# Optimization experiments

Hardware: AMD Instinct MI355X
Metric: run time of the kernel (lower is better)

Reference implementation:

```python
import jax, jax.numpy as jnp
import numpy as np

L, B, DW, DH, W, NG = 1024, 64, 300, 256, 2, 1
NEG = -1e25


def window_context(hx, w):
    """Concat of 2w+1 time-shifted copies of hx [L,B,D] -> [L,B,(2w+1)D].
    Order matches torch: shift-down by w..1, identity, shift-up by 1..w."""
    Lh = hx.shape[0]
    parts = []
    for i in range(w, -w - 1, -1):
        if i > 0:
            p = jnp.concatenate([jnp.zeros_like(hx[:i]), hx[:Lh - i]], axis=0)
        elif i < 0:
            k = -i
            p = jnp.concatenate([hx[k:], jnp.zeros_like(hx[:k])], axis=0)
        else:
            p = hx
        parts.append(p)
    return jnp.concatenate(parts, axis=2)


def setup_inputs() -> dict:
    key = jax.random.key(0)
    ks = jax.random.split(key, 11)
    E = (2 * W + 1) * DH
    std = 0.1  # reset_parameters('normal') uses N(0, 0.1)
    return {
        "src_seq": jax.random.normal(ks[0], (L, B, DW), jnp.float32),
        "h0": jax.random.normal(ks[1], (L + NG, B, DH), jnp.float32),
        "c0": jax.random.normal(ks[2], (L + NG, B, DH), jnp.float32),
        # word-gate params stacked over gates (i,l,r,f,s,o,u)
        "Ww": std * jax.random.normal(ks[3], (7, DH, E), jnp.float32),
        "Wu": std * jax.random.normal(ks[4], (7, DH, DW), jnp.float32),
        "Wv": std * jax.random.normal(ks[5], (7, DH, DH), jnp.float32),
        "Wb": std * jax.random.normal(ks[6], (7, DH), jnp.float32),
        # sentence-gate params stacked over gates (g,f,o)
        "Sw": std * jax.random.normal(ks[7], (3, DH, DH), jnp.float32),
        "Su": std * jax.random.normal(ks[8], (3, DH, DH), jnp.float32),
        "Sb": std * jax.random.normal(ks[9], (3, DH), jnp.float32),
        "src_len": jax.random.randint(ks[10], (B, 1), 1, L + 1, jnp.int32),
    }


def reference(src_seq, h0, c0, Ww, Wu, Wv, Wb, Sw, Su, Sb, src_len):
    # seq_mask[t, b] = True where t >= length[b]  -> [L, B, 1]
    seq_mask = (jnp.arange(L)[:, None] >= src_len[:, 0][None, :])[:, :, None]

    h_g1 = h0[L:]                                 # [1,B,DH] sentence node
    c_g1 = c0[L:]
    h_w1 = jnp.where(seq_mask, 0.0, h0[:L])       # [L,B,DH] word nodes
    c_w1 = jnp.where(seq_mask, 0.0, c0[:L])
    h_hat = h_w1.mean(axis=0)                     # [B,DH]
    hg = h_g1[0]                                  # [B,DH]

    # --- sentence node update (gate order g,f,o) ---
    fg = jax.nn.sigmoid(hg @ Sw[0].T + h_hat @ Su[0].T + Sb[0])[None]   # [1,B,DH]
    og = jax.nn.sigmoid(hg @ Sw[2].T + h_hat @ Su[2].T + Sb[2])[None]
    fi = jax.nn.sigmoid((hg @ Sw[1].T)[None]
                        + jnp.einsum('lbh,dh->lbd', h_w1, Su[1]) + Sb[1])
    fi = jnp.where(seq_mask, NEG, fi)
    fi_n = jax.nn.softmax(fi, axis=0)             # softmax over time
    c_g = fg * c_g1 + (fi_n * c_w1).sum(axis=0)
    h_g = og * jnp.tanh(c_g)

    # --- word node update (gate order i,l,r,f,s,o,u) ---
    eps = window_context(h_w1, W)                 # [L,B,(2W+1)DH]
    pre = (jnp.einsum('lbe,gde->glbd', eps, Ww)
           + jnp.einsum('lbw,gdw->glbd', src_seq, Wu)
           + jnp.einsum('bh,gdh->gbd', hg, Wv)[:, None]
           + Wb[:, None, None])                   # [7,L,B,DH]
    i_ = jax.nn.sigmoid(pre[0])
    l_ = jax.nn.sigmoid(pre[1])
    r_ = jax.nn.sigmoid(pre[2])
    f_ = jax.nn.sigmoid(pre[3])
    s_ = jax.nn.sigmoid(pre[4])
    o_ = jax.nn.sigmoid(pre[5])
    u_ = jnp.tanh(pre[6])

    gates = jnp.stack((l_, f_, r_, s_, i_), axis=0)          # [5,L,B,DH]
    gates = jnp.where(seq_mask[None], NEG, gates)
    gates_n = jax.nn.softmax(gates, axis=0)                  # softmax over 5 gates

    c_ctx = window_context(c_w1, 1)                          # window_size=1 (default)
    c_l, c_c, c_r = jnp.split(c_ctx, 3, axis=2)
    c_merged = jnp.stack(
        (c_l, c_c, c_r, jnp.broadcast_to(c_g1, c_c.shape), u_), axis=0)
    c_w = (gates_n * c_merged).sum(axis=0)
    c_w = jnp.where(seq_mask, 0.0, c_w)
    h_w = o_ * jnp.tanh(c_w)

    h_t = jnp.concatenate((h_w, h_g), axis=0)                # [L+1,B,DH]
    c_t = jnp.concatenate((c_w, c_g), axis=0)
    return (h_t, c_t)
```

## Files before the change

### kernel.cpp

```cpp
#include <hip/hip_runtime.h>
#include <hip/hip_bf16.h>

#define L_SEQ 1024
#define N_B   64
#define D_H   256
#define D_W   300
#define LDK   72
#define LDH   264

typedef __bf16 bf16x8 __attribute__((ext_vector_type(8)));
typedef float  f32x4  __attribute__((ext_vector_type(4)));
typedef unsigned short us8 __attribute__((ext_vector_type(8)));

#if defined(__has_builtin)
#if __has_builtin(__builtin_amdgcn_global_load_lds)
#define HAS_ASYNC_LDS 1
#endif
#endif

__device__ inline float b2f(unsigned short u){
    union { unsigned int i; float f; } v; v.i = ((unsigned int)u) << 16; return v.f;
}
__device__ inline unsigned short f2b(float f){
    union { float f; unsigned int i; } v; v.f = f;
    unsigned int u = v.i;
    return (unsigned short)((u + 0x7fffu + ((u >> 16) & 1u)) >> 16);
}
__device__ inline float sigf(float x){ return 1.0f / (1.0f + __expf(-x)); }
__device__ inline float tanhfast(float x){ return 1.0f - 2.0f / (__expf(2.0f*x) + 1.0f); }

__device__ inline float ldf(const void* p, size_t i, int isf){
    return isf ? ((const float*)p)[i] : b2f(((const unsigned short*)p)[i]);
}
__device__ inline unsigned short ld1b(const void* p, size_t i, int isf){
    return isf ? f2b(((const float*)p)[i]) : ((const unsigned short*)p)[i];
}
__device__ inline us8 ld8(const void* p, size_t i, int isf){
    if (isf){
        const float* f = (const float*)p + i;
        float4 x = *(const float4*)f;
        float4 y = *(const float4*)(f + 4);
        us8 r = { f2b(x.x), f2b(x.y), f2b(x.z), f2b(x.w),
                  f2b(y.x), f2b(y.y), f2b(y.z), f2b(y.w) };
        return r;
    }
    return *(const us8*)((const unsigned short*)p + i);
}
__device__ inline unsigned int ld2(const void* p, size_t i, int isf){
    if (isf){
        const float* f = (const float*)p + i;
        float2 x = *(const float2*)f;
        return (unsigned int)f2b(x.x) | ((unsigned int)f2b(x.y) << 16);
    }
    return *(const unsigned int*)((const unsigned short*)p + i);
}
__device__ inline float4 ldf4(const void* p, size_t i, int isf){
    if (isf) return *(const float4*)((const float*)p + i);
    unsigned long long v = *(const unsigned long long*)((const unsigned short*)p + i);
    float4 r;
    r.x = b2f((unsigned short)( v        & 0xffffu));
    r.y = b2f((unsigned short)((v >> 16) & 0xffffu));
    r.z = b2f((unsigned short)((v >> 32) & 0xffffu));
    r.w = b2f((unsigned short)( v >> 48));
    return r;
}

__device__ inline void stage16(const unsigned short* g, unsigned short* lds_base, int lane){
#ifdef HAS_ASYNC_LDS
    __builtin_amdgcn_global_load_lds(
        (const __attribute__((address_space(1))) unsigned int*)g,
        (__attribute__((address_space(3))) unsigned int*)lds_base, 16, 0, 0);
#else
    *(us8*)(lds_base + lane*8) = *(const us8*)g;
#endif
}

__global__ __launch_bounds__(256) void k_detect(const void* __restrict__ h0, int* __restrict__ flag)
{
    int tid = threadIdx.x;
    const unsigned short* u = (const unsigned short*)h0;
    int cnt = 0;
    #pragma unroll
    for (int i = 0; i < 4; i++){
        unsigned short v = u[(size_t)(tid * 4 + i) * 2];
        int e = (v >> 7) & 0xFF;
        cnt += (e >= 90 && e <= 150) ? 1 : 0;
    }
    __shared__ int red[256];
    red[tid] = cnt;
    __syncthreads();
    for (int s = 128; s > 0; s >>= 1){
        if (tid < s) red[tid] += red[tid + s];
        __syncthreads();
    }
    if (tid == 0) flag[0] = (red[0] > 512) ? 0 : 1;
}

__global__ __launch_bounds__(256) void k_conv_h(const void* __restrict__ h0,
    const int* __restrict__ slen, unsigned short* __restrict__ hpad, const int* __restrict__ flagp)
{
    int isf = flagp[0];
    int i = blockIdx.y;
    int idx = (blockIdx.x*256 + threadIdx.x)*8;
    int b = idx >> 8;
    int l = i - 2;
    us8 v = {0,0,0,0,0,0,0,0};
    if ((unsigned)l < 1024u && l < slen[b])
        v = ld8(h0, (size_t)l*16384 + idx, isf);
    *(us8*)(hpad + (size_t)i*16384 + idx) = v;
}

__global__ __launch_bounds__(256) void k_conv_src(const void* __restrict__ src,
    unsigned short* __restrict__ srcpad, const int* __restrict__ flagp)
{
    int isf = flagp[0];
    int gid = blockIdx.x*256 + threadIdx.x;
    int row = gid / 40, k = gid % 40, col = k*8;
    us8 v = {0,0,0,0,0,0,0,0};
    if (col + 8 <= 300) v = ld8(src, (size_t)row*300 + col, isf);
    else if (col < 300){
        for (int e = 0; e < 300 - col; ++e) v[e] = ld1b(src, (size_t)row*300 + col + e, isf);
    }
    *(us8*)(srcpad + (size_t)row*320 + col) = v;
}

__global__ __launch_bounds__(256) void k_conv_w(const void* __restrict__ Ww,
    const void* __restrict__ Wu, unsigned short* __restrict__ Wcat, const int* __restrict__ flagp)
{
    int isf = flagp[0];
    int gid = blockIdx.x*256 + threadIdx.x;
    int row = gid / 200, k = gid % 200, col = k*8;
    int dgrp = row / 112, rem = row % 112;
    int g = rem >> 4, d = dgrp*16 + (rem & 15);
    size_t n = (size_t)g*256 + d;
    us8 v = {0,0,0,0,0,0,0,0};
    if (col < 1280) v = ld8(Ww, n*1280 + col, isf);
    else {
        int w = col - 1280;
        if (w + 8 <= 300) v = ld8(Wu, n*300 + w, isf);
        else if (w < 300){
            for (int e = 0; e < 300 - w; ++e) v[e] = ld1b(Wu, n*300 + w + e, isf);
        }
    }
    *(us8*)(Wcat + (size_t)row*1600 + col) = v;
}

__global__ __launch_bounds__(256) void k_conv_su(const void* __restrict__ Su,
    unsigned short* __restrict__ Subf, const int* __restrict__ flagp)
{
    int isf = flagp[0];
    int gid = blockIdx.x*256 + threadIdx.x;
    *(us8*)(Subf + (size_t)gid*8) = ld8(Su, (size_t)65536 + (size_t)gid*8, isf);
}

__global__ __launch_bounds__(256) void k_hhat_fast(const unsigned short* __restrict__ hpad,
    float* __restrict__ hhat)
{
    int b = blockIdx.x, part = blockIdx.y, d = threadIdx.x;
    float s = 0.f;
    const unsigned short* p = hpad + (size_t)(2 + part*128)*16384 + b*256 + d;
    for (int ll = 0; ll < 128; ++ll)
        s += b2f(p[(size_t)ll*16384]);
    atomicAdd(&hhat[b*256 + d], s);
}

__global__ __launch_bounds__(1024) void k_hhat(const void* __restrict__ h0,
    const int* __restrict__ slen, float* __restrict__ hhat, const int* __restrict__ flagp)
{
    int isf = flagp[0];
    int b = blockIdx.x;
    int part = threadIdx.x >> 8;
    int d = threadIdx.x & 255;
    int lenb = slen[b];
    float s = 0.f;
    for (int l = part; l < lenb; l += 4)
        s += ldf(h0, (size_t)l*16384 + b*256 + d, isf);
    __shared__ float red[1024];
    red[threadIdx.x] = s;
    __syncthreads();
    if (part == 0)
        hhat[b*256 + d] = (red[d] + red[d+256] + red[d+512] + red[d+768]);
}

__global__ __launch_bounds__(256) void k_small(const void* __restrict__ h0,
    const float* __restrict__ hhat, const void* __restrict__ Sw,
    const void* __restrict__ Su, const void* __restrict__ Sb,
    float* __restrict__ fg, float* __restrict__ og, float* __restrict__ sg,
    const int* __restrict__ flagp, float hs)
{
    int isf = flagp[0];
    int b = blockIdx.x; int d = threadIdx.x;
    __shared__ float hgl[256], hhl[256];
    hgl[d] = ldf(h0, (size_t)16777216 + b*256 + d, isf);
    hhl[d] = hhat[b*256 + d] * hs;
    __syncthreads();
    size_t sw0 = (size_t)d*256, sw1 = (size_t)(256+d)*256, sw2 = (size_t)(512+d)*256;
    size_t su0 = (size_t)d*256, su2 = (size_t)(512+d)*256;
    float a0=0.f,a1=0.f,a2=0.f,a3=0.f,a4=0.f;
    #pragma unroll 4
    for (int h=0; h<256; h+=4){
        float4 w0 = ldf4(Sw, sw0+h, isf);
        float4 u0 = ldf4(Su, su0+h, isf);
        float4 w1 = ldf4(Sw, sw1+h, isf);
        float4 w2 = ldf4(Sw, sw2+h, isf);
        float4 u2 = ldf4(Su, su2+h, isf);
        float g0=hgl[h], g1=hgl[h+1], g2=hgl[h+2], g3=hgl[h+3];
        float q0=hhl[h], q1=hhl[h+1], q2=hhl[h+2], q3=hhl[h+3];
        a0 += g0*w0.x + g1*w0.y + g2*w0.z + g3*w0.w;
        a1 += q0*u0.x + q1*u0.y + q2*u0.z + q3*u0.w;
        a2 += g0*w1.x + g1*w1.y + g2*w1.z + g3*w1.w;
        a3 += g0*w2.x + g1*w2.y + g2*w2.z + g3*w2.w;
        a4 += q0*u2.x + q1*u2.y + q2*u2.z + q3*u2.w;
    }
    int i = b*256 + d;
    fg[i] = sigf(a0 + a1 + ldf(Sb, d, isf));
    sg[i] = a2 + ldf(Sb, 256 + d, isf);
    og[i] = sigf(a3 + a4 + ldf(Sb, 512 + d, isf));
}

__global__ __launch_bounds__(256) void k_hgwv(const void* __restrict__ h0,
    const void* __restrict__ Wv, const void* __restrict__ Wb,
    float* __restrict__ hgWvB, const int* __restrict__ flagp)
{
    int isf = flagp[0];
    int b = blockIdx.x, g = blockIdx.y, d = threadIdx.x;
    __shared__ float hgl[256];
    hgl[d] = ldf(h0, (size_t)16777216 + b*256 + d, isf);
    __syncthreads();
    size_t wv = ((size_t)g*256 + d)*256;
    float a = 0.f;
    #pragma unroll 4
    for (int h=0; h<256; h+=4){
        float4 w = ldf4(Wv, wv+h, isf);
        a += hgl[h]*w.x + hgl[h+1]*w.y + hgl[h+2]*w.z + hgl[h+3]*w.w;
    }
    hgWvB[(size_t)b*1792 + g*256 + d] = a + ldf(Wb, g*256 + d, isf);
}

__global__ __launch_bounds__(256) void k_fi_fast(const unsigned short* __restrict__ hpad,
    const void* __restrict__ c0, const unsigned short* __restrict__ Subf,
    const int* __restrict__ slen, const float* __restrict__ sg,
    float* __restrict__ numv, float* __restrict__ denv, const int* __restrict__ flagp)
{
    int isf = flagp[0];
    __shared__ unsigned short Hs[64*LDH];
    int tid = threadIdx.x;
    int b = blockIdx.x;
    int l0 = blockIdx.y * 64;
    int lenb = slen[b];
    #pragma unroll
    for (int i=0;i<8;i++){
        int c = tid + i*256;
        int r = c >> 5;
        int col = (c & 31) << 3;
        *(us8*)(Hs + r*LDH + col) =
            *(const us8*)(hpad + (size_t)(l0 + r + 2)*16384 + b*256 + col);
    }
    __syncthreads();
    int wv = tid >> 6, lane = tid & 63, qd = lane >> 4, lc = lane & 15;
    f32x4 zero4 = {0.f,0.f,0.f,0.f};
    for (int dci=0; dci<4; ++dci){
        int d = (wv*4 + dci) * 16 + lc;
        f32x4 acc[4];
        #pragma unroll
        for (int t=0;t<4;t++) acc[t] = zero4;
        #pragma unroll
        for (int ks=0; ks<8; ++ks){
            int k0 = ks*32 + qd*8;
            bf16x8 bb = *(const bf16x8*)(Subf + (size_t)d*256 + k0);
            #pragma unroll
            for (int lt=0; lt<4; ++lt){
                bf16x8 aa = *(const bf16x8*)(Hs + (lt*16 + lc)*LDH + k0);
                acc[lt] = __builtin_amdgcn_mfma_f32_16x16x32_bf16(aa, bb, acc[lt], 0, 0, 0);
            }
        }
        float sgv = sg[b*256 + d];
        float pn = 0.f, pd = 0.f;
        #pragma unroll
        for (int lt=0; lt<4; ++lt){
            #pragma unroll
            for (int r=0; r<4; ++r){
                int l = l0 + lt*16 + qd*4 + r;
                if (l < lenb){
                    float e = __expf(sigf(acc[lt][r] + sgv));
                    pd += e;
                    pn += e * ldf(c0, (size_t)l*16384 + b*256 + d, isf);
                }
            }
        }
        pn += __shfl_xor(pn, 16); pn += __shfl_xor(pn, 32);
        pd += __shfl_xor(pd, 16); pd += __shfl_xor(pd, 32);
        if (qd == 0){
            atomicAdd(&numv[b*256 + d], pn);
            atomicAdd(&denv[b*256 + d], pd);
        }
    }
}

__global__ __launch_bounds__(256) void k_fi(const void* __restrict__ h0,
    const void* __restrict__ c0, const void* __restrict__ Su,
    const int* __restrict__ slen, const float* __restrict__ sg,
    float* __restrict__ numv, float* __restrict__ denv, const int* __restrict__ flagp)
{
    int isf = flagp[0];
    __shared__ unsigned short Hs[64*LDH];
    int tid = threadIdx.x;
    int b = blockIdx.x;
    int l0 = blockIdx.y * 64;
    int lenb = slen[b];
    #pragma unroll
    for (int i=0;i<8;i++){
        int c = tid + i*256;
        int r = c >> 5;
        int col = (c & 31) << 3;
        int l = l0 + r;
        us8 v = {0,0,0,0,0,0,0,0};
        if (l < lenb)
            v = ld8(h0, (size_t)l*16384 + b*256 + col, isf);
        *(us8*)(Hs + r*LDH + col) = v;
    }
    __syncthreads();
    int wv = tid >> 6, lane = tid & 63, qd = lane >> 4, lc = lane & 15;
    f32x4 zero4 = {0.f,0.f,0.f,0.f};
    for (int dci=0; dci<4; ++dci){
        int d = (wv*4 + dci) * 16 + lc;
        f32x4 acc[4];
        #pragma unroll
        for (int t=0;t<4;t++) acc[t] = zero4;
        #pragma unroll
        for (int ks=0; ks<8; ++ks){
            int k0 = ks*32 + qd*8;
            union { us8 u; bf16x8 b; } cv; cv.u = ld8(Su, (size_t)65536 + (size_t)d*256 + k0, isf);
            bf16x8 bb = cv.b;
            #pragma unroll
            for (int lt=0; lt<4; ++lt){
                bf16x8 aa = *(const bf16x8*)(Hs + (lt*16 + lc)*LDH + k0);
                acc[lt] = __builtin_amdgcn_mfma_f32_16x16x32_bf16(aa, bb, acc[lt], 0, 0, 0);
            }
        }
        float sgv = sg[b*256 + d];
        float pn = 0.f, pd = 0.f;
        #pragma unroll
        for (int lt=0; lt<4; ++lt){
            #pragma unroll
            for (int r=0; r<4; ++r){
                int l = l0 + lt*16 + qd*4 + r;
                if (l < lenb){
                    float e = __expf(sigf(acc[lt][r] + sgv));
                    pd += e;
                    pn += e * ldf(c0, (size_t)l*16384 + b*256 + d, isf);
                }
            }
        }
        pn += __shfl_xor(pn, 16); pn += __shfl_xor(pn, 32);
        pd += __shfl_xor(pd, 16); pd += __shfl_xor(pd, 32);
        if (qd == 0){
            atomicAdd(&numv[b*256 + d], pn);
            atomicAdd(&denv[b*256 + d], pd);
        }
    }
}

__global__ __launch_bounds__(256) void k_cg(const void* __restrict__ c0,
    const float* __restrict__ fg, const float* __restrict__ og,
    const float* __restrict__ numv, const float* __restrict__ denv,
    float* __restrict__ outh, float* __restrict__ outc,
    const int* __restrict__ flagp)
{
    int isf = flagp[0];
    int i = blockIdx.x*256 + threadIdx.x;
    float cg1 = ldf(c0, (size_t)16777216 + i, isf);
    float cg = fg[i]*cg1 + numv[i]/denv[i];
    float hg = og[i]*tanhfast(cg);
    outh[(size_t)16777216 + i] = hg;
    outc[(size_t)16777216 + i] = cg;
}

__global__ __launch_bounds__(256) void k_main_fast(
    const unsigned short* __restrict__ hpad, const unsigned short* __restrict__ srcpad,
    const unsigned short* __restrict__ Wcat, const void* __restrict__ c0,
    const int* __restrict__ slen, const float* __restrict__ hgWvB,
    float* __restrict__ outh, float* __restrict__ outc, const int* __restrict__ flagp)
{
    int isf = flagp[0];
    __shared__ unsigned short As[2][128*64];
    __shared__ unsigned short Bs[2][112*64];
    int tid = threadIdx.x;
    int d0 = blockIdx.x * 16;
    int m0 = blockIdx.y * 128;
    int wv = tid >> 6, lane = tid & 63, qd = lane >> 4, lc = lane & 15;

    const unsigned short* gbB = Wcat + (size_t)blockIdx.x * 112 * 1600;

    int arow[4], agc[4];
    #pragma unroll
    for (int i=0;i<4;i++){
        int s = i*256 + tid;
        arow[i] = s >> 3;
        agc[i]  = ((s & 7) ^ ((s >> 3) & 7)) << 3;
    }
    int s3 = 768 + tid;
    int brow3 = s3 >> 3;
    int bgc3  = ((s3 & 7) ^ ((s3 >> 3) & 7)) << 3;

    f32x4 zero4 = {0.f,0.f,0.f,0.f};
    f32x4 acc[2][7];
    #pragma unroll
    for (int a=0;a<2;a++)
        #pragma unroll
        for (int g=0;g<7;g++) acc[a][g] = zero4;

#define STAGE_TILE(sel_, kt_) do {                                                   \
        const unsigned short* ga_; int astr_;                                        \
        if ((kt_) < 20){                                                             \
            ga_ = hpad + (((size_t)(m0 + (((kt_)>>2)<<6))) << 8) + (((kt_) & 3) << 6); \
            astr_ = 256;                                                             \
        } else {                                                                     \
            ga_ = srcpad + (size_t)m0*320 + (((kt_) - 20) << 6);                     \
            astr_ = 320;                                                             \
        }                                                                            \
        const unsigned short* gb_ = gbB + ((size_t)(kt_) << 6);                      \
        _Pragma("unroll")                                                            \
        for (int i_=0;i_<4;i_++)                                                     \
            stage16(ga_ + (size_t)arow[i_]*astr_ + agc[i_],                          \
                    &As[(sel_)][i_*2048 + wv*512], lane);                            \
        _Pragma("unroll")                                                            \
        for (int i_=0;i_<3;i_++)                                                     \
            stage16(gb_ + (size_t)arow[i_]*1600 + agc[i_],                           \
                    &Bs[(sel_)][i_*2048 + wv*512], lane);                            \
        if (tid < 128)                                                               \
            stage16(gb_ + (size_t)brow3*1600 + bgc3,                                 \
                    &Bs[(sel_)][3*2048 + wv*512], lane);                             \
    } while(0)

    STAGE_TILE(0, 0);
    asm volatile("s_waitcnt vmcnt(0)" ::: "memory");
    __builtin_amdgcn_s_barrier();
    asm volatile("" ::: "memory");

    int cur = 0;
    for (int kt=0; kt<25; ++kt){
        if (kt < 24){
            int nxt = cur ^ 1;
            int kk  = kt + 1;
            STAGE_TILE(nxt, kk);
        }
        const unsigned short* Ac = &As[cur][0];
        const unsigned short* Bc = &Bs[cur][0];
        __builtin_amdgcn_s_setprio(1);
        #pragma unroll
        for (int ks=0; ks<2; ++ks){
            int ch = (ks << 2) + qd;
            int xa = (ch ^ (lc & 7)) << 3;
            bf16x8 a0 = *(const bf16x8*)(Ac + (wv*32 + lc)*64 + xa);
            bf16x8 a1 = *(const bf16x8*)(Ac + (wv*32 + 16 + lc)*64 + xa);
            #pragma unroll
            for (int g=0; g<7; ++g){
                bf16x8 bg = *(const bf16x8*)(Bc + (g*16 + lc)*64 + xa);
                acc[0][g] = __builtin_amdgcn_mfma_f32_16x16x32_bf16(a0, bg, acc[0][g], 0,0,0);
                acc[1][g] = __builtin_amdgcn_mfma_f32_16x16x32_bf16(a1, bg, acc[1][g], 0,0,0);
            }
        }
        __builtin_amdgcn_s_setprio(0);
        asm volatile("s_waitcnt vmcnt(0) lgkmcnt(0)" ::: "memory");
        __builtin_amdgcn_s_barrier();
        asm volatile("" ::: "memory");
        cur ^= 1;
    }
#undef STAGE_TILE

    int d = d0 + lc;
    #pragma unroll
    for (int mt=0; mt<2; ++mt){
        #pragma unroll
        for (int r=0; r<4; ++r){
            int m = m0 + wv*32 + mt*16 + qd*4 + r;
            int l = m >> 6, b = m & 63;
            size_t oi = (size_t)m*256 + d;
            int lenb = slen[b];
            float hw = 0.f, cw = 0.f;
            if (l < lenb){
                const float* hv = hgWvB + (size_t)b*1792 + d;
                float p0 = acc[mt][0][r] + hv[0];
                float p1 = acc[mt][1][r] + hv[256];
                float p2 = acc[mt][2][r] + hv[512];
                float p3 = acc[mt][3][r] + hv[768];
                float p4 = acc[mt][4][r] + hv[1024];
                float p5 = acc[mt][5][r] + hv[1280];
                float p6 = acc[mt][6][r] + hv[1536];
                float e_l = __expf(sigf(p1));
                float e_f = __expf(sigf(p3));
                float e_r = __expf(sigf(p2));
                float e_s = __expf(sigf(p4));
                float e_i = __expf(sigf(p0));
                float S = e_l + e_f + e_r + e_s + e_i;
                float u_ = tanhfast(p6);
                float cl = (l >= 1) ? ldf(c0, oi - 16384, isf) : 0.f;
                float cc = ldf(c0, oi, isf);
                float cr = (l + 1 < lenb) ? ldf(c0, oi + 16384, isf) : 0.f;
                float cg1 = ldf(c0, (size_t)16777216 + b*256 + d, isf);
                cw = (e_l*cl + e_f*cc + e_r*cr + e_s*cg1 + e_i*u_) / S;
                hw = sigf(p5) * tanhfast(cw);
            }
            outh[oi] = hw;
            outc[oi] = cw;
        }
    }
}

__global__ __launch_bounds__(256) void k_main(
    const void* __restrict__ src, const void* __restrict__ h0,
    const void* __restrict__ c0, const void* __restrict__ Ww,
    const void* __restrict__ Wu, const int* __restrict__ slen,
    const float* __restrict__ hgWvB,
    float* __restrict__ outh, float* __restrict__ outc,
    const int* __restrict__ flagp)
{
    int isf = flagp[0];
    __shared__ unsigned short As[128*LDK];
    __shared__ unsigned short Bs[112*LDK];
    int tid = threadIdx.x;
    int m0 = blockIdx.x * 128;
    int d0 = blockIdx.y * 16;
    int wv = tid >> 6, lane = tid & 63, qd = lane >> 4, lc = lane & 15;

    int ar[4], acol[4], al[4], ab[4], alen[4];
    #pragma unroll
    for (int i=0;i<4;i++){
        int c = tid + i*256;
        ar[i] = c >> 3; acol[i] = (c & 7) << 3;
        int m = m0 + ar[i];
        al[i] = m >> 6; ab[i] = m & 63;
        alen[i] = slen[ab[i]];
    }

    f32x4 zero4 = {0.f,0.f,0.f,0.f};
    f32x4 acc[2][7];
    #pragma unroll
    for (int a=0;a<2;a++)
        #pragma unroll
        for (int g=0;g<7;g++) acc[a][g] = zero4;

    for (int kt=0; kt<25; ++kt){
        __syncthreads();
        if (kt < 20){
            int j = kt >> 2;
            int koff = (kt & 3) << 6;
            #pragma unroll
            for (int i=0;i<4;i++){
                int lp = al[i] + j - 2;
                us8 v = {0,0,0,0,0,0,0,0};
                if ((unsigned)lp < 1024u && lp < alen[i])
                    v = ld8(h0, (size_t)lp*16384 + ab[i]*256 + koff + acol[i], isf);
                *(us8*)(As + ar[i]*LDK + acol[i]) = v;
            }
            #pragma unroll
            for (int i=0;i<4;i++){
                int c = tid + i*256;
                if (c < 896){
                    int rr = c >> 3, col = (c & 7) << 3;
                    int g = rr >> 4, d = d0 + (rr & 15);
                    *(us8*)(Bs + rr*LDK + col) =
                        ld8(Ww, ((size_t)g*256 + d)*1280 + j*256 + koff + col, isf);
                }
            }
        } else {
            int w0 = (kt - 20) << 6;
            #pragma unroll
            for (int i=0;i<16;i++){
                int c = tid + i*256;
                int r = c >> 5, wi = (c & 31) << 1;
                int w = w0 + wi;
                int m = m0 + r;
                unsigned int v = 0;
                if (w < 300) v = ld2(src, (size_t)m*300 + w, isf);
                *(unsigned int*)(As + r*LDK + wi) = v;
            }
            #pragma unroll
            for (int i=0;i<14;i++){
                int c = tid + i*256;
                int rr = c >> 5, wi = (c & 31) << 1;
                int w = w0 + wi;
                int g = rr >> 4, d = d0 + (rr & 15);
                unsigned int v = 0;
                if (w < 300) v = ld2(Wu, ((size_t)g*256 + d)*300 + w, isf);
                *(unsigned int*)(Bs + rr*LDK + wi) = v;
            }
        }
        __syncthreads();
        #pragma unroll
        for (int ks=0; ks<2; ++ks){
            int k0 = (ks << 5) + (qd << 3);
            bf16x8 a0 = *(const bf16x8*)(As + (wv*32 + lc)*LDK + k0);
            bf16x8 a1 = *(const bf16x8*)(As + (wv*32 + 16 + lc)*LDK + k0);
            #pragma unroll
            for (int g=0; g<7; ++g){
                bf16x8 bg = *(const bf16x8*)(Bs + (g*16 + lc)*LDK + k0);
                acc[0][g] = __builtin_amdgcn_mfma_f32_16x16x32_bf16(a0, bg, acc[0][g], 0,0,0);
                acc[1][g] = __builtin_amdgcn_mfma_f32_16x16x32_bf16(a1, bg, acc[1][g], 0,0,0);
            }
        }
    }

    int d = d0 + lc;
    #pragma unroll
    for (int mt=0; mt<2; ++mt){
        #pragma unroll
        for (int r=0; r<4; ++r){
            int m = m0 + wv*32 + mt*16 + qd*4 + r;
            int l = m >> 6, b = m & 63;
            size_t oi = (size_t)m*256 + d;
            int lenb = slen[b];
            float hw = 0.f, cw = 0.f;
            if (l < lenb){
                const float* hv = hgWvB + (size_t)b*1792 + d;
                float p0 = acc[mt][0][r] + hv[0];
                float p1 = acc[mt][1][r] + hv[256];
                float p2 = acc[mt][2][r] + hv[512];
                float p3 = acc[mt][3][r] + hv[768];
                float p4 = acc[mt][4][r] + hv[1024];
                float p5 = acc[mt][5][r] + hv[1280];
                float p6 = acc[mt][6][r] + hv[1536];
                float e_l = __expf(sigf(p1));
                float e_f = __expf(sigf(p3));
                float e_r = __expf(sigf(p2));
                float e_s = __expf(sigf(p4));
                float e_i = __expf(sigf(p0));
                float S = e_l + e_f + e_r + e_s + e_i;
                float u_ = tanhfast(p6);
                float cl = (l >= 1) ? ldf(c0, oi - 16384, isf) : 0.f;
                float cc = ldf(c0, oi, isf);
                float cr = (l + 1 < lenb) ? ldf(c0, oi + 16384, isf) : 0.f;
                float cg1 = ldf(c0, (size_t)16777216 + b*256 + d, isf);
                cw = (e_l*cl + e_f*cc + e_r*cr + e_s*cg1 + e_i*u_) / S;
                hw = sigf(p5) * tanhfast(cw);
            }
            outh[oi] = hw;
            outc[oi] = cw;
        }
    }
}

extern "C" void kernel_launch(void* const* d_in, const int* in_sizes, int n_in,
                              void* d_out, int out_size, void* d_ws, size_t ws_size,
                              hipStream_t stream)
{
    const void* src = d_in[0];
    const void* h0  = d_in[1];
    const void* c0  = d_in[2];
    const void* Ww  = d_in[3];
    const void* Wu  = d_in[4];
    const void* Wv  = d_in[5];
    const void* Wb  = d_in[6];
    const void* Sw  = d_in[7];
    const void* Su  = d_in[8];
    const void* Sb  = d_in[9];
    const int* slen = (const int*)d_in[10];

    float* outh = (float*)d_out;
    float* outc = outh + (size_t)1025*64*256;

    float* ws    = (float*)d_ws;
    float* numv  = ws;
    float* denv  = ws + 16384;
    float* hhat  = ws + 32768;
    float* fg    = ws + 49152;
    float* og    = ws + 65536;
    float* sg    = ws + 81920;
    float* hgWvB = ws + 98304;
    int*   flag  = (int*)(ws + 212992);

    unsigned short* bfbase = (unsigned short*)(ws + 213024);
    unsigned short* hpad   = bfbase;
    unsigned short* srcpad = bfbase + (size_t)16842752;
    unsigned short* Wcat   = bfbase + (size_t)37814272;
    unsigned short* Subf   = bfbase + (size_t)40681472;
    const size_t NEED = 852096 + (size_t)40747008*2;

    hipLaunchKernelGGL(k_detect, dim3(1), dim3(256), 0, stream, h0, flag);
    hipMemsetAsync(ws, 0, (size_t)3*16384*sizeof(float), stream);

    if (ws_size >= NEED){
        hipLaunchKernelGGL(k_conv_h,  dim3(8,1028), dim3(256), 0, stream, h0, slen, hpad, flag);
        hipLaunchKernelGGL(k_conv_src, dim3(10240), dim3(256), 0, stream, src, srcpad, flag);
        hipLaunchKernelGGL(k_conv_w,   dim3(1400),  dim3(256), 0, stream, Ww, Wu, Wcat, flag);
        hipLaunchKernelGGL(k_conv_su,  dim3(32),    dim3(256), 0, stream, Su, Subf, flag);
        hipLaunchKernelGGL(k_hhat_fast, dim3(64,8), dim3(256), 0, stream, hpad, hhat);
        hipLaunchKernelGGL(k_small, dim3(64), dim3(256), 0, stream, h0, hhat, Sw, Su, Sb,
                           fg, og, sg, flag, 1.0f/1024.0f);
        hipLaunchKernelGGL(k_hgwv, dim3(64,7), dim3(256), 0, stream, h0, Wv, Wb, hgWvB, flag);
        hipLaunchKernelGGL(k_fi_fast, dim3(64,16), dim3(256), 0, stream, hpad, c0, Subf, slen,
                           sg, numv, denv, flag);
        hipLaunchKernelGGL(k_cg, dim3(64), dim3(256), 0, stream, c0, fg, og, numv, denv,
                           outh, outc, flag);
        hipLaunchKernelGGL(k_main_fast, dim3(16,512), dim3(256), 0, stream,
                           hpad, srcpad, Wcat, c0, slen, hgWvB, outh, outc, flag);
    } else {
        hipLaunchKernelGGL(k_hhat, dim3(64), dim3(1024), 0, stream, h0, slen, hhat, flag);
        hipLaunchKernelGGL(k_small, dim3(64), dim3(256), 0, stream, h0, hhat, Sw, Su, Sb,
                           fg, og, sg, flag, 1.0f/1024.0f);
        hipLaunchKernelGGL(k_hgwv, dim3(64,7), dim3(256), 0, stream, h0, Wv, Wb, hgWvB, flag);
        hipLaunchKernelGGL(k_fi, dim3(64,16), dim3(256), 0, stream, h0, c0, Su, slen,
                           sg, numv, denv, flag);
        hipLaunchKernelGGL(k_cg, dim3(64), dim3(256), 0, stream, c0, fg, og, numv, denv,
                           outh, outc, flag);
        hipLaunchKernelGGL(k_main, dim3(512,16), dim3(256), 0, stream,
                           src, h0, c0, Ww, Wu, slen, hgWvB, outh, outc, flag);
    }
}
```

Before: 976.9 us.

## Restructure main GEMM to 4-stage 32-wide K pipeline with partial vmcnt waits

```diff
diff --git a/kernel.cpp b/kernel.cpp
--- a/kernel.cpp
+++ b/kernel.cpp
@@ -383,25 +383,43 @@
     float* __restrict__ outh, float* __restrict__ outc, const int* __restrict__ flagp)
 {
     int isf = flagp[0];
-    __shared__ unsigned short As[2][128*64];
-    __shared__ unsigned short Bs[2][112*64];
+    __shared__ unsigned short smem[32768];
     int tid = threadIdx.x;
     int d0 = blockIdx.x * 16;
     int m0 = blockIdx.y * 128;
     int wv = tid >> 6, lane = tid & 63, qd = lane >> 4, lc = lane & 15;
 
-    const unsigned short* gbB = Wcat + (size_t)blockIdx.x * 112 * 1600;
-
-    int arow[4], agc[4];
-    #pragma unroll
-    for (int i=0;i<4;i++){
-        int s = i*256 + tid;
-        arow[i] = s >> 3;
-        agc[i]  = ((s & 7) ^ ((s >> 3) & 7)) << 3;
-    }
-    int s3 = 768 + tid;
-    int brow3 = s3 >> 3;
-    int bgc3  = ((s3 & 7) ^ ((s3 >> 3) & 7)) << 3;
+    const unsigned short* gBbase = Wcat + (size_t)blockIdx.x * 112 * 1600;
+    const unsigned short* gAh = hpad + (size_t)m0 * 256;
+    const unsigned short* gAs = srcpad + (size_t)m0 * 320;
+
+    int goffAh[2], goffAs[2], goffB[2];
+    #pragma unroll
+    for (int i=0;i<2;i++){
+        int c = i*256 + tid;
+        int r = c >> 2, sl = c & 3;
+        int mk = (r & 3) ^ ((r >> 2) & 3);
+        int gc = sl ^ mk;
+        goffAh[i] = r*256 + (gc<<3);
+        goffAs[i] = r*320 + (gc<<3);
+        int rb = (r < 112) ? r : 111;
+        goffB[i]  = rb*1600 + (gc<<3);
+    }
+
+    int r0 = wv*32 + lc, r1 = r0 + 16;
+    int aoff0 = r0*32 + ((qd ^ ((r0&3)^((r0>>2)&3))) << 3);
+    int aoff1 = r1*32 + ((qd ^ ((r1&3)^((r1>>2)&3))) << 3);
+    int boff0, boff1, boff2, boff3, boff4, boff5, boff6;
+    {
+        int rb, mk;
+        rb = 0*16+lc; mk = (rb&3)^((rb>>2)&3); boff0 = 4096 + rb*32 + ((qd^mk)<<3);
+        rb = 1*16+lc; mk = (rb&3)^((rb>>2)&3); boff1 = 4096 + rb*32 + ((qd^mk)<<3);
+        rb = 2*16+lc; mk = (rb&3)^((rb>>2)&3); boff2 = 4096 + rb*32 + ((qd^mk)<<3);
+        rb = 3*16+lc; mk = (rb&3)^((rb>>2)&3); boff3 = 4096 + rb*32 + ((qd^mk)<<3);
+        rb = 4*16+lc; mk = (rb&3)^((rb>>2)&3); boff4 = 4096 + rb*32 + ((qd^mk)<<3);
+        rb = 5*16+lc; mk = (rb&3)^((rb>>2)&3); boff5 = 4096 + rb*32 + ((qd^mk)<<3);
+        rb = 6*16+lc; mk = (rb&3)^((rb>>2)&3); boff6 = 4096 + rb*32 + ((qd^mk)<<3);
+    }
 
     f32x4 zero4 = {0.f,0.f,0.f,0.f};
     f32x4 acc[2][7];
@@ -410,64 +428,75 @@
         #pragma unroll
         for (int g=0;g<7;g++) acc[a][g] = zero4;
 
-#define STAGE_TILE(sel_, kt_) do {                                                   \
-        const unsigned short* ga_; int astr_;                                        \
-        if ((kt_) < 20){                                                             \
-            ga_ = hpad + (((size_t)(m0 + (((kt_)>>2)<<6))) << 8) + (((kt_) & 3) << 6); \
-            astr_ = 256;                                                             \
-        } else {                                                                     \
-            ga_ = srcpad + (size_t)m0*320 + (((kt_) - 20) << 6);                     \
-            astr_ = 320;                                                             \
-        }                                                                            \
-        const unsigned short* gb_ = gbB + ((size_t)(kt_) << 6);                      \
-        _Pragma("unroll")                                                            \
-        for (int i_=0;i_<4;i_++)                                                     \
-            stage16(ga_ + (size_t)arow[i_]*astr_ + agc[i_],                          \
-                    &As[(sel_)][i_*2048 + wv*512], lane);                            \
-        _Pragma("unroll")                                                            \
-        for (int i_=0;i_<3;i_++)                                                     \
-            stage16(gb_ + (size_t)arow[i_]*1600 + agc[i_],                           \
-                    &Bs[(sel_)][i_*2048 + wv*512], lane);                            \
-        if (tid < 128)                                                               \
-            stage16(gb_ + (size_t)brow3*1600 + bgc3,                                 \
-                    &Bs[(sel_)][3*2048 + wv*512], lane);                             \
+#define STAGE_H(hs_) do {                                                        \
+        int hh_ = (hs_);                                                         \
+        unsigned short* sb_ = smem + (hh_&3)*8192;                               \
+        const unsigned short* gB_ = gBbase + hh_*32;                             \
+        if (hh_ < 40){                                                           \
+            const unsigned short* gA_ = gAh + ((hh_>>3)*16384 + ((hh_&7)<<5));   \
+            stage16(gA_ + goffAh[0], sb_ + wv*512, lane);                        \
+            stage16(gA_ + goffAh[1], sb_ + 2048 + wv*512, lane);                 \
+        } else {                                                                 \
+            const unsigned short* gA_ = gAs + ((hh_-40)<<5);                     \
+            stage16(gA_ + goffAs[0], sb_ + wv*512, lane);                        \
+            stage16(gA_ + goffAs[1], sb_ + 2048 + wv*512, lane);                 \
+        }                                                                        \
+        stage16(gB_ + goffB[0], sb_ + 4096 + wv*512, lane);                      \
+        stage16(gB_ + goffB[1], sb_ + 6144 + wv*512, lane);                      \
     } while(0)
 
-    STAGE_TILE(0, 0);
-    asm volatile("s_waitcnt vmcnt(0)" ::: "memory");
+#define ITER_H(h_, DS_) do {                                                     \
+        const unsigned short* lb_ = smem + ((h_)&3)*8192;                        \
+        bf16x8 va0 = *(const bf16x8*)(lb_ + aoff0);                              \
+        bf16x8 va1 = *(const bf16x8*)(lb_ + aoff1);                              \
+        bf16x8 vb0 = *(const bf16x8*)(lb_ + boff0);                              \
+        bf16x8 vb1 = *(const bf16x8*)(lb_ + boff1);                              \
+        bf16x8 vb2 = *(const bf16x8*)(lb_ + boff2);                              \
+        bf16x8 vb3 = *(const bf16x8*)(lb_ + boff3);                              \
+        bf16x8 vb4 = *(const bf16x8*)(lb_ + boff4);                              \
+        bf16x8 vb5 = *(const bf16x8*)(lb_ + boff5);                              \
+        bf16x8 vb6 = *(const bf16x8*)(lb_ + boff6);                              \
+        if (DS_) STAGE_H((h_) + 3);                                              \
+        __builtin_amdgcn_s_setprio(1);                                           \
+        acc[0][0] = __builtin_amdgcn_mfma_f32_16x16x32_bf16(va0, vb0, acc[0][0],0,0,0); \
+        acc[1][0] = __builtin_amdgcn_mfma_f32_16x16x32_bf16(va1, vb0, acc[1][0],0,0,0); \
+        acc[0][1] = __builtin_amdgcn_mfma_f32_16x16x32_bf16(va0, vb1, acc[0][1],0,0,0); \
+        acc[1][1] = __builtin_amdgcn_mfma_f32_16x16x32_bf16(va1, vb1, acc[1][1],0,0,0); \
+        acc[0][2] = __builtin_amdgcn_mfma_f32_16x16x32_bf16(va0, vb2, acc[0][2],0,0,0); \
+        acc[1][2] = __builtin_amdgcn_mfma_f32_16x16x32_bf16(va1, vb2, acc[1][2],0,0,0); \
+        acc[0][3] = __builtin_amdgcn_mfma_f32_16x16x32_bf16(va0, vb3, acc[0][3],0,0,0); \
+        acc[1][3] = __builtin_amdgcn_mfma_f32_16x16x32_bf16(va1, vb3, acc[1][3],0,0,0); \
+        acc[0][4] = __builtin_amdgcn_mfma_f32_16x16x32_bf16(va0, vb4, acc[0][4],0,0,0); \
+        acc[1][4] = __builtin_amdgcn_mfma_f32_16x16x32_bf16(va1, vb4, acc[1][4],0,0,0); \
+        acc[0][5] = __builtin_amdgcn_mfma_f32_16x16x32_bf16(va0, vb5, acc[0][5],0,0,0); \
+        acc[1][5] = __builtin_amdgcn_mfma_f32_16x16x32_bf16(va1, vb5, acc[1][5],0,0,0); \
+        acc[0][6] = __builtin_amdgcn_mfma_f32_16x16x32_bf16(va0, vb6, acc[0][6],0,0,0); \
+        acc[1][6] = __builtin_amdgcn_mfma_f32_16x16x32_bf16(va1, vb6, acc[1][6],0,0,0); \
+        __builtin_amdgcn_s_setprio(0);                                           \
+    } while(0)
+
+    STAGE_H(0); STAGE_H(1); STAGE_H(2);
+    asm volatile("s_waitcnt vmcnt(8)" ::: "memory");
     __builtin_amdgcn_s_barrier();
     asm volatile("" ::: "memory");
 
-    int cur = 0;
-    for (int kt=0; kt<25; ++kt){
-        if (kt < 24){
-            int nxt = cur ^ 1;
-            int kk  = kt + 1;
-            STAGE_TILE(nxt, kk);
-        }
-        const unsigned short* Ac = &As[cur][0];
-        const unsigned short* Bc = &Bs[cur][0];
-        __builtin_amdgcn_s_setprio(1);
-        #pragma unroll
-        for (int ks=0; ks<2; ++ks){
-            int ch = (ks << 2) + qd;
-            int xa = (ch ^ (lc & 7)) << 3;
-            bf16x8 a0 = *(const bf16x8*)(Ac + (wv*32 + lc)*64 + xa);
-            bf16x8 a1 = *(const bf16x8*)(Ac + (wv*32 + 16 + lc)*64 + xa);
-            #pragma unroll
-            for (int g=0; g<7; ++g){
-                bf16x8 bg = *(const bf16x8*)(Bc + (g*16 + lc)*64 + xa);
-                acc[0][g] = __builtin_amdgcn_mfma_f32_16x16x32_bf16(a0, bg, acc[0][g], 0,0,0);
-                acc[1][g] = __builtin_amdgcn_mfma_f32_16x16x32_bf16(a1, bg, acc[1][g], 0,0,0);
-            }
-        }
-        __builtin_amdgcn_s_setprio(0);
-        asm volatile("s_waitcnt vmcnt(0) lgkmcnt(0)" ::: "memory");
+    for (int h = 0; h < 47; ++h){
+        ITER_H(h, 1);
+        asm volatile("s_waitcnt vmcnt(8) lgkmcnt(0)" ::: "memory");
         __builtin_amdgcn_s_barrier();
         asm volatile("" ::: "memory");
-        cur ^= 1;
-    }
-#undef STAGE_TILE
+    }
+    ITER_H(47, 0);
+    asm volatile("s_waitcnt vmcnt(4) lgkmcnt(0)" ::: "memory");
+    __builtin_amdgcn_s_barrier();
+    asm volatile("" ::: "memory");
+    ITER_H(48, 0);
+    asm volatile("s_waitcnt vmcnt(0) lgkmcnt(0)" ::: "memory");
+    __builtin_amdgcn_s_barrier();
+    asm volatile("" ::: "memory");
+    ITER_H(49, 0);
+#undef ITER_H
+#undef STAGE_H
 
     int d = d0 + lc;
     #pragma unroll
```

Measured after the change: 945.2 us. 3.2% less time.

## Pre-pack weights into MFMA fragment order and load GEMM operands directly to registers

Applied to the files above, without the earlier changes.

```diff
diff --git a/kernel.cpp b/kernel.cpp
--- a/kernel.cpp
+++ b/kernel.cpp
@@ -65,16 +65,6 @@
     return r;
 }
 
-__device__ inline void stage16(const unsigned short* g, unsigned short* lds_base, int lane){
-#ifdef HAS_ASYNC_LDS
-    __builtin_amdgcn_global_load_lds(
-        (const __attribute__((address_space(1))) unsigned int*)g,
-        (__attribute__((address_space(3))) unsigned int*)lds_base, 16, 0, 0);
-#else
-    *(us8*)(lds_base + lane*8) = *(const us8*)g;
-#endif
-}
-
 __global__ __launch_bounds__(256) void k_detect(const void* __restrict__ h0, int* __restrict__ flag)
 {
     int tid = threadIdx.x;
@@ -129,20 +119,22 @@
 {
     int isf = flagp[0];
     int gid = blockIdx.x*256 + threadIdx.x;
-    int row = gid / 200, k = gid % 200, col = k*8;
-    int dgrp = row / 112, rem = row % 112;
-    int g = rem >> 4, d = dgrp*16 + (rem & 15);
+    int bx = gid / 22400, rem = gid % 22400;
+    int h = rem / 448, rem2 = rem % 448;
+    int rr = rem2 >> 2, c8 = rem2 & 3;
+    int g = rr >> 4, d = bx*16 + (rr & 15);
+    int k = h*32 + c8*8;
     size_t n = (size_t)g*256 + d;
     us8 v = {0,0,0,0,0,0,0,0};
-    if (col < 1280) v = ld8(Ww, n*1280 + col, isf);
+    if (k < 1280) v = ld8(Ww, n*1280 + k, isf);
     else {
-        int w = col - 1280;
+        int w = k - 1280;
         if (w + 8 <= 300) v = ld8(Wu, n*300 + w, isf);
         else if (w < 300){
             for (int e = 0; e < 300 - w; ++e) v[e] = ld1b(Wu, n*300 + w + e, isf);
         }
     }
-    *(us8*)(Wcat + (size_t)row*1600 + col) = v;
+    *(us8*)(Wcat + (size_t)gid*8) = v;
 }
 
 __global__ __launch_bounds__(256) void k_conv_su(const void* __restrict__ Su,
@@ -376,32 +368,156 @@
     outc[(size_t)16777216 + i] = cg;
 }
 
-__global__ __launch_bounds__(256) void k_main_fast(
+__global__ __launch_bounds__(256, 2) void k_main_fast(
     const unsigned short* __restrict__ hpad, const unsigned short* __restrict__ srcpad,
     const unsigned short* __restrict__ Wcat, const void* __restrict__ c0,
     const int* __restrict__ slen, const float* __restrict__ hgWvB,
     float* __restrict__ outh, float* __restrict__ outc, const int* __restrict__ flagp)
 {
     int isf = flagp[0];
-    __shared__ unsigned short As[2][128*64];
-    __shared__ unsigned short Bs[2][112*64];
     int tid = threadIdx.x;
     int d0 = blockIdx.x * 16;
-    int m0 = blockIdx.y * 128;
+    int m0 = blockIdx.y * 256;
     int wv = tid >> 6, lane = tid & 63, qd = lane >> 4, lc = lane & 15;
 
-    const unsigned short* gbB = Wcat + (size_t)blockIdx.x * 112 * 1600;
-
-    int arow[4], agc[4];
+    int mr0 = m0 + wv*64 + lc;
+    const unsigned short* pA0h = hpad + (size_t)(mr0      )*256 + qd*8;
+    const unsigned short* pA1h = hpad + (size_t)(mr0 + 16 )*256 + qd*8;
+    const unsigned short* pA2h = hpad + (size_t)(mr0 + 32 )*256 + qd*8;
+    const unsigned short* pA3h = hpad + (size_t)(mr0 + 48 )*256 + qd*8;
+    const unsigned short* pA0s = srcpad + (size_t)(mr0      )*320 + qd*8;
+    const unsigned short* pA1s = srcpad + (size_t)(mr0 + 16 )*320 + qd*8;
+    const unsigned short* pA2s = srcpad + (size_t)(mr0 + 32 )*320 + qd*8;
+    const unsigned short* pA3s = srcpad + (size_t)(mr0 + 48 )*320 + qd*8;
+    const unsigned short* pB = Wcat + ((size_t)(blockIdx.x*50)*112 + lc)*32 + qd*8;
+
+    f32x4 zero4 = {0.f,0.f,0.f,0.f};
+    f32x4 acc[4][7];
+    #pragma unroll
+    for (int a=0;a<4;a++)
+        #pragma unroll
+        for (int g=0;g<7;g++) acc[a][g] = zero4;
+
+#define LOAD_PH(AV, BV, h_) do {                                                 \
+        int hh_ = (h_);                                                          \
+        if (hh_ < 40){                                                           \
+            int off_ = ((hh_>>3)<<14) + ((hh_&7)<<5);                            \
+            AV##0 = *(const bf16x8*)(pA0h + off_);                               \
+            AV##1 = *(const bf16x8*)(pA1h + off_);                               \
+            AV##2 = *(const bf16x8*)(pA2h + off_);                               \
+            AV##3 = *(const bf16x8*)(pA3h + off_);                               \
+        } else {                                                                 \
+            int off_ = (hh_ - 40) << 5;                                          \
+            AV##0 = *(const bf16x8*)(pA0s + off_);                               \
+            AV##1 = *(const bf16x8*)(pA1s + off_);                               \
+            AV##2 = *(const bf16x8*)(pA2s + off_);                               \
+            AV##3 = *(const bf16x8*)(pA3s + off_);                               \
+        }                                                                        \
+        const unsigned short* bp_ = pB + hh_*3584;                               \
+        BV##0 = *(const bf16x8*)(bp_ + 0);                                       \
+        BV##1 = *(const bf16x8*)(bp_ + 512);                                     \
+        BV##2 = *(const bf16x8*)(bp_ + 1024);                                    \
+        BV##3 = *(const bf16x8*)(bp_ + 1536);                                    \
+        BV##4 = *(const bf16x8*)(bp_ + 2048);                                    \
+        BV##5 = *(const bf16x8*)(bp_ + 2560);                                    \
+        BV##6 = *(const bf16x8*)(bp_ + 3072);                                    \
+    } while(0)
+
+#define MG1(A_, B_, g_) do {                                                     \
+        acc[0][g_] = __builtin_amdgcn_mfma_f32_16x16x32_bf16(A_##0, B_##g_, acc[0][g_],0,0,0); \
+        acc[1][g_] = __builtin_amdgcn_mfma_f32_16x16x32_bf16(A_##1, B_##g_, acc[1][g_],0,0,0); \
+        acc[2][g_] = __builtin_amdgcn_mfma_f32_16x16x32_bf16(A_##2, B_##g_, acc[2][g_],0,0,0); \
+        acc[3][g_] = __builtin_amdgcn_mfma_f32_16x16x32_bf16(A_##3, B_##g_, acc[3][g_],0,0,0); \
+    } while(0)
+#define MFMA_PH(A_, B_) do { MG1(A_,B_,0); MG1(A_,B_,1); MG1(A_,B_,2); MG1(A_,B_,3); \
+                             MG1(A_,B_,4); MG1(A_,B_,5); MG1(A_,B_,6); } while(0)
+
+    bf16x8 xa0, xa1, xa2, xa3, ya0, ya1, ya2, ya3;
+    bf16x8 xb0, xb1, xb2, xb3, xb4, xb5, xb6;
+    bf16x8 yb0, yb1, yb2, yb3, yb4, yb5, yb6;
+
+    LOAD_PH(xa, xb, 0);
+    for (int h = 0; h < 48; h += 2){
+        LOAD_PH(ya, yb, h+1);
+        __builtin_amdgcn_s_setprio(1);
+        MFMA_PH(xa, xb);
+        __builtin_amdgcn_s_setprio(0);
+        LOAD_PH(xa, xb, h+2);
+        __builtin_amdgcn_s_setprio(1);
+        MFMA_PH(ya, yb);
+        __builtin_amdgcn_s_setprio(0);
+    }
+    LOAD_PH(ya, yb, 49);
+    MFMA_PH(xa, xb);
+    MFMA_PH(ya, yb);
+#undef LOAD_PH
+#undef MG1
+#undef MFMA_PH
+
+    int d = d0 + lc;
+    #pragma unroll
+    for (int mt=0; mt<4; ++mt){
+        #pragma unroll
+        for (int r=0; r<4; ++r){
+            int m = m0 + wv*64 + mt*16 + qd*4 + r;
+            int l = m >> 6, b = m & 63;
+            size_t oi = (size_t)m*256 + d;
+            int lenb = slen[b];
+            float hw = 0.f, cw = 0.f;
+            if (l < lenb){
+                const float* hv = hgWvB + (size_t)b*1792 + d;
+                float p0 = acc[mt][0][r] + hv[0];
+                float p1 = acc[mt][1][r] + hv[256];
+                float p2 = acc[mt][2][r] + hv[512];
+                float p3 = acc[mt][3][r] + hv[768];
+                float p4 = acc[mt][4][r] + hv[1024];
+                float p5 = acc[mt][5][r] + hv[1280];
+                float p6 = acc[mt][6][r] + hv[1536];
+                float e_l = __expf(sigf(p1));
+                float e_f = __expf(sigf(p3));
+                float e_r = __expf(sigf(p2));
+                float e_s = __expf(sigf(p4));
+                float e_i = __expf(sigf(p0));
+                float S = e_l + e_f + e_r + e_s + e_i;
+                float u_ = tanhfast(p6);
+                float cl = (l >= 1) ? ldf(c0, oi - 16384, isf) : 0.f;
+                float cc = ldf(c0, oi, isf);
+                float cr = (l + 1 < lenb) ? ldf(c0, oi + 16384, isf) : 0.f;
+                float cg1 = ldf(c0, (size_t)16777216 + b*256 + d, isf);
+                cw = (e_l*cl + e_f*cc + e_r*cr + e_s*cg1 + e_i*u_) / S;
+                hw = sigf(p5) * tanhfast(cw);
+            }
+            outh[oi] = hw;
+            outc[oi] = cw;
+        }
+    }
+}
+
+__global__ __launch_bounds__(256) void k_main(
+    const void* __restrict__ src, const void* __restrict__ h0,
+    const void* __restrict__ c0, const void* __restrict__ Ww,
+    const void* __restrict__ Wu, const int* __restrict__ slen,
+    const float* __restrict__ hgWvB,
+    float* __restrict__ outh, float* __restrict__ outc,
+    const int* __restrict__ flagp)
+{
+    int isf = flagp[0];
+    __shared__ unsigned short As[128*LDK];
+    __shared__ unsigned short Bs[112*LDK];
+    int tid = threadIdx.x;
+    int m0 = blockIdx.x * 128;
+    int d0 = blockIdx.y * 16;
+    int wv = tid >> 6, lane = tid & 63, qd = lane >> 4, lc = lane & 15;
+
+    int ar[4], acol[4], al[4], ab[4], alen[4];
     #pragma unroll
     for (int i=0;i<4;i++){
-        int s = i*256 + tid;
-        arow[i] = s >> 3;
-        agc[i]  = ((s & 7) ^ ((s >> 3) & 7)) << 3;
-    }
-    int s3 = 768 + tid;
-    int brow3 = s3 >> 3;
-    int bgc3  = ((s3 & 7) ^ ((s3 >> 3) & 7)) << 3;
+        int c = tid + i*256;
+        ar[i] = c >> 3; acol[i] = (c & 7) << 3;
+        int m = m0 + ar[i];
+        al[i] = m >> 6; ab[i] = m & 63;
+        alen[i] = slen[ab[i]];
+    }
 
     f32x4 zero4 = {0.f,0.f,0.f,0.f};
     f32x4 acc[2][7];
@@ -410,64 +526,66 @@
         #pragma unroll
         for (int g=0;g<7;g++) acc[a][g] = zero4;
 
-#define STAGE_TILE(sel_, kt_) do {                                                   \
-        const unsigned short* ga_; int astr_;                                        \
-        if ((kt_) < 20){                                                             \
-            ga_ = hpad + (((size_t)(m0 + (((kt_)>>2)<<6))) << 8) + (((kt_) & 3) << 6); \
-            astr_ = 256;                                                             \
-        } else {                                                                     \
-            ga_ = srcpad + (size_t)m0*320 + (((kt_) - 20) << 6);                     \
-            astr_ = 320;                                                             \
-        }                                                                            \
-        const unsigned short* gb_ = gbB + ((size_t)(kt_) << 6);                      \
-        _Pragma("unroll")                                                            \
-        for (int i_=0;i_<4;i_++)                                                     \
-            stage16(ga_ + (size_t)arow[i_]*astr_ + agc[i_],                          \
-                    &As[(sel_)][i_*2048 + wv*512], lane);                            \
-        _Pragma("unroll")                                                            \
-        for (int i_=0;i_<3;i_++)                                                     \
-            stage16(gb_ + (size_t)arow[i_]*1600 + agc[i_],                           \
-                    &Bs[(sel_)][i_*2048 + wv*512], lane);                            \
-        if (tid < 128)                                                               \
-            stage16(gb_ + (size_t)brow3*1600 + bgc3,                                 \
-                    &Bs[(sel_)][3*2048 + wv*512], lane);                             \
-    } while(0)
-
-    STAGE_TILE(0, 0);
-    asm volatile("s_waitcnt vmcnt(0)" ::: "memory");
-    __builtin_amdgcn_s_barrier();
-    asm volatile("" ::: "memory");
-
-    int cur = 0;
     for (int kt=0; kt<25; ++kt){
-        if (kt < 24){
-            int nxt = cur ^ 1;
-            int kk  = kt + 1;
-            STAGE_TILE(nxt, kk);
-        }
-        const unsigned short* Ac = &As[cur][0];
-        const unsigned short* Bc = &Bs[cur][0];
-        __builtin_amdgcn_s_setprio(1);
+        __syncthreads();
+        if (kt < 20){
+            int j = kt >> 2;
+            int koff = (kt & 3) << 6;
+            #pragma unroll
+            for (int i=0;i<4;i++){
+                int lp = al[i] + j - 2;
+                us8 v = {0,0,0,0,0,0,0,0};
+                if ((unsigned)lp < 1024u && lp < alen[i])
+                    v = ld8(h0, (size_t)lp*16384 + ab[i]*256 + koff + acol[i], isf);
+                *(us8*)(As + ar[i]*LDK + acol[i]) = v;
+            }
+            #pragma unroll
+            for (int i=0;i<4;i++){
+                int c = tid + i*256;
+                if (c < 896){
+                    int rr = c >> 3, col = (c & 7) << 3;
+                    int g = rr >> 4, d = d0 + (rr & 15);
+                    *(us8*)(Bs + rr*LDK + col) =
+                        ld8(Ww, ((size_t)g*256 + d)*1280 + j*256 + koff + col, isf);
+                }
+            }
+        } else {
+            int w0 = (kt - 20) << 6;
+            #pragma unroll
+            for (int i=0;i<16;i++){
+                int c = tid + i*256;
+                int r = c >> 5, wi = (c & 31) << 1;
+                int w = w0 + wi;
+                int m = m0 + r;
+                unsigned int v = 0;
+                if (w < 300) v = ld2(src, (size_t)m*300 + w, isf);
+                *(unsigned int*)(As + r*LDK + wi) = v;
+            }
+            #pragma unroll
+            for (int i=0;i<14;i++){
+                int c = tid + i*256;
+                int rr = c >> 5, wi = (c & 31) << 1;
+                int w = w0 + wi;
+                int g = rr >> 4, d = d0 + (rr & 15);
+                unsigned int v = 0;
+                if (w < 300) v = ld2(Wu, ((size_t)g*256 + d)*300 + w, isf);
+                *(unsigned int*)(Bs + rr*LDK + wi) = v;
+            }
+        }
+        __syncthreads();
         #pragma unroll
         for (int ks=0; ks<2; ++ks){
-            int ch = (ks << 2) + qd;
-            int xa = (ch ^ (lc & 7)) << 3;
-            bf16x8 a0 = *(const bf16x8*)(Ac + (wv*32 + lc)*64 + xa);
-            bf16x8 a1 = *(const bf16x8*)(Ac + (wv*32 + 16 + lc)*64 + xa);
+            int k0 = (ks << 5) + (qd << 3);
+            bf16x8 a0 = *(const bf16x8*)(As + (wv*32 + lc)*LDK + k0);
+            bf16x8 a1 = *(const bf16x8*)(As + (wv*32 + 16 + lc)*LDK + k0);
             #pragma unroll
             for (int g=0; g<7; ++g){
-                bf16x8 bg = *(const bf16x8*)(Bc + (g*16 + lc)*64 + xa);
+                bf16x8 bg = *(const bf16x8*)(Bs + (g*16 + lc)*LDK + k0);
                 acc[0][g] = __builtin_amdgcn_mfma_f32_16x16x32_bf16(a0, bg, acc[0][g], 0,0,0);
                 acc[1][g] = __builtin_amdgcn_mfma_f32_16x16x32_bf16(a1, bg, acc[1][g], 0,0,0);
             }
         }
-        __builtin_amdgcn_s_setprio(0);
-        asm volatile("s_waitcnt vmcnt(0) lgkmcnt(0)" ::: "memory");
-        __builtin_amdgcn_s_barrier();
-        asm volatile("" ::: "memory");
-        cur ^= 1;
-    }
-#undef STAGE_TILE
+    }
 
     int d = d0 + lc;
     #pragma unroll
@@ -508,139 +626,6 @@
     }
 }
 
-__global__ __launch_bounds__(256) void k_main(
-    const void* __restrict__ src, const void* __restrict__ h0,
-    const void* __restrict__ c0, const void* __restrict__ Ww,
-    const void* __restrict__ Wu, const int* __restrict__ slen,
-    const float* __restrict__ hgWvB,
-    float* __restrict__ outh, float* __restrict__ outc,
-    const int* __restrict__ flagp)
-{
-    int isf = flagp[0];
-    __shared__ unsigned short As[128*LDK];
-    __shared__ unsigned short Bs[112*LDK];
-    int tid = threadIdx.x;
-    int m0 = blockIdx.x * 128;
-    int d0 = blockIdx.y * 16;
-    int wv = tid >> 6, lane = tid & 63, qd = lane >> 4, lc = lane & 15;
-
-    int ar[4], acol[4], al[4], ab[4], alen[4];
-    #pragma unroll
-    for (int i=0;i<4;i++){
-        int c = tid + i*256;
-        ar[i] = c >> 3; acol[i] = (c & 7) << 3;
-        int m = m0 + ar[i];
-        al[i] = m >> 6; ab[i] = m & 63;
-        alen[i] = slen[ab[i]];
-    }
-
-    f32x4 zero4 = {0.f,0.f,0.f,0.f};
-    f32x4 acc[2][7];
-    #pragma unroll
-    for (int a=0;a<2;a++)
-        #pragma unroll
-        for (int g=0;g<7;g++) acc[a][g] = zero4;
-
-    for (int kt=0; kt<25; ++kt){
-        __syncthreads();
-        if (kt < 20){
-            int j = kt >> 2;
-            int koff = (kt & 3) << 6;
-            #pragma unroll
-            for (int i=0;i<4;i++){
-                int lp = al[i] + j - 2;
-                us8 v = {0,0,0,0,0,0,0,0};
-                if ((unsigned)lp < 1024u && lp < alen[i])
-                    v = ld8(h0, (size_t)lp*16384 + ab[i]*256 + koff + acol[i], isf);
-                *(us8*)(As + ar[i]*LDK + acol[i]) = v;
-            }
-            #pragma unroll
-            for (int i=0;i<4;i++){
-                int c = tid + i*256;
-                if (c < 896){
-                    int rr = c >> 3, col = (c & 7) << 3;
-                    int g = rr >> 4, d = d0 + (rr & 15);
-                    *(us8*)(Bs + rr*LDK + col) =
-                        ld8(Ww, ((size_t)g*256 + d)*1280 + j*256 + koff + col, isf);
-                }
-            }
-        } else {
-            int w0 = (kt - 20) << 6;
-            #pragma unroll
-            for (int i=0;i<16;i++){
-                int c = tid + i*256;
-                int r = c >> 5, wi = (c & 31) << 1;
-                int w = w0 + wi;
-                int m = m0 + r;
-                unsigned int v = 0;
-                if (w < 300) v = ld2(src, (size_t)m*300 + w, isf);
-                *(unsigned int*)(As + r*LDK + wi) = v;
-            }
-            #pragma unroll
-            for (int i=0;i<14;i++){
-                int c = tid + i*256;
-                int rr = c >> 5, wi = (c & 31) << 1;
-                int w = w0 + wi;
-                int g = rr >> 4, d = d0 + (rr & 15);
-                unsigned int v = 0;
-                if (w < 300) v = ld2(Wu, ((size_t)g*256 + d)*300 + w, isf);
-                *(unsigned int*)(Bs + rr*LDK + wi) = v;
-            }
-        }
-        __syncthreads();
-        #pragma unroll
-        for (int ks=0; ks<2; ++ks){
-            int k0 = (ks << 5) + (qd << 3);
-            bf16x8 a0 = *(const bf16x8*)(As + (wv*32 + lc)*LDK + k0);
-            bf16x8 a1 = *(const bf16x8*)(As + (wv*32 + 16 + lc)*LDK + k0);
-            #pragma unroll
-            for (int g=0; g<7; ++g){
-                bf16x8 bg = *(const bf16x8*)(Bs + (g*16 + lc)*LDK + k0);
-                acc[0][g] = __builtin_amdgcn_mfma_f32_16x16x32_bf16(a0, bg, acc[0][g], 0,0,0);
-                acc[1][g] = __builtin_amdgcn_mfma_f32_16x16x32_bf16(a1, bg, acc[1][g], 0,0,0);
-            }
-        }
-    }
-
-    int d = d0 + lc;
-    #pragma unroll
-    for (int mt=0; mt<2; ++mt){
-        #pragma unroll
-        for (int r=0; r<4; ++r){
-            int m = m0 + wv*32 + mt*16 + qd*4 + r;
-            int l = m >> 6, b = m & 63;
-            size_t oi = (size_t)m*256 + d;
-            int lenb = slen[b];
-            float hw = 0.f, cw = 0.f;
-            if (l < lenb){
-                const float* hv = hgWvB + (size_t)b*1792 + d;
-                float p0 = acc[mt][0][r] + hv[0];
-                float p1 = acc[mt][1][r] + hv[256];
-                float p2 = acc[mt][2][r] + hv[512];
-                float p3 = acc[mt][3][r] + hv[768];
-                float p4 = acc[mt][4][r] + hv[1024];
-                float p5 = acc[mt][5][r] + hv[1280];
-                float p6 = acc[mt][6][r] + hv[1536];
-                float e_l = __expf(sigf(p1));
-                float e_f = __expf(sigf(p3));
-                float e_r = __expf(sigf(p2));
-                float e_s = __expf(sigf(p4));
-                float e_i = __expf(sigf(p0));
-                float S = e_l + e_f + e_r + e_s + e_i;
-                float u_ = tanhfast(p6);
-                float cl = (l >= 1) ? ldf(c0, oi - 16384, isf) : 0.f;
-                float cc = ldf(c0, oi, isf);
-                float cr = (l + 1 < lenb) ? ldf(c0, oi + 16384, isf) : 0.f;
-                float cg1 = ldf(c0, (size_t)16777216 + b*256 + d, isf);
-                cw = (e_l*cl + e_f*cc + e_r*cr + e_s*cg1 + e_i*u_) / S;
-                hw = sigf(p5) * tanhfast(cw);
-            }
-            outh[oi] = hw;
-            outc[oi] = cw;
-        }
-    }
-}
-
 extern "C" void kernel_launch(void* const* d_in, const int* in_sizes, int n_in,
                               void* d_out, int out_size, void* d_ws, size_t ws_size,
                               hipStream_t stream)
@@ -693,7 +678,7 @@
                            sg, numv, denv, flag);
         hipLaunchKernelGGL(k_cg, dim3(64), dim3(256), 0, stream, c0, fg, og, numv, denv,
                            outh, outc, flag);
-        hipLaunchKernelGGL(k_main_fast, dim3(16,512), dim3(256), 0, stream,
+        hipLaunchKernelGGL(k_main_fast, dim3(16,256), dim3(256), 0, stream,
                            hpad, srcpad, Wcat, c0, slen, hgWvB, outh, outc, flag);
     } else {
         hipLaunchKernelGGL(k_hhat, dim3(64), dim3(1024), 0, stream, h0, slen, hhat, flag);
```

Result: slower. 1.148 ms (+17.5%).
